# Kernel optimization log

Measured on AMD Instinct MI355X. Metric: run time of the kernel, lower is better.

## Reference

```python
import jax, jax.numpy as jnp
import numpy as np

B, N, F = 4, 1024, 512        # batch, tokens, features
H, D = 8, 64                  # heads, attention_dim (= value dim here)
E = 16                        # edge feature dim
LN_EPS = 1e-5


def setup_inputs() -> dict:
    key = jax.random.key(0)
    ks = jax.random.split(key, 9)
    receiver_input = jax.random.normal(ks[0], (B, N, F), dtype=jnp.float32)
    edge_features = jax.random.normal(ks[1], (B, N, N, E), dtype=jnp.float32)
    mask = (jax.random.uniform(ks[2], (B, N, N)) > 0.5).astype(jnp.float32)
    s = 1.0 / np.sqrt(F)
    Wq = jax.random.normal(ks[3], (F, H * D), dtype=jnp.float32) * s
    Wk = jax.random.normal(ks[4], (F, H * D), dtype=jnp.float32) * s
    Wv = jax.random.normal(ks[5], (F, H * D), dtype=jnp.float32) * s
    We = jax.random.normal(ks[6], (E, H), dtype=jnp.float32) * (1.0 / np.sqrt(E))
    Wo = jax.random.normal(ks[7], (H * D, H * D), dtype=jnp.float32) * (1.0 / np.sqrt(H * D))
    ln_scale = jnp.ones((F,), dtype=jnp.float32)
    ln_offset = jnp.zeros((F,), dtype=jnp.float32)
    return {
        "receiver_input": receiver_input, "edge_features": edge_features,
        "mask": mask, "ln_scale": ln_scale, "ln_offset": ln_offset,
        "Wq": Wq, "Wk": Wk, "Wv": Wv, "We": We, "Wo": Wo,
    }


def _layer_norm(x, scale, offset):
    mu = jnp.mean(x, axis=-1, keepdims=True)
    var = jnp.var(x, axis=-1, keepdims=True)
    return (x - mu) * jax.lax.rsqrt(var + LN_EPS) * scale + offset


def reference(receiver_input, edge_features, mask, ln_scale, ln_offset, Wq, Wk, Wv, We, Wo):
    r = _layer_norm(receiver_input, ln_scale, ln_offset)   # sender = receiver (self-attn)
    q = (r @ Wq).reshape(B, N, H, D)
    k = (r @ Wk).reshape(B, N, H, D)
    v = (r @ Wv).reshape(B, N, H, D)
    # logits [b, i, j, h]; edge bias added BEFORE softmax (over senders j = axis -2)
    logits = jnp.einsum("bihf,bjhf->bijh", q, k) + edge_features @ We
    w = jax.nn.softmax(logits, axis=-2)
    w = w * mask[..., None]                                 # post-softmax mask multiply
    out = jnp.einsum("bijh,bjhv->bihv", w, v)
    out = out.reshape(B, N, H * D) * (1.0 / jnp.sqrt(jnp.float32(D)))
    out = out @ Wo
    out = out + receiver_input                              # residual (shapes match: F == H*D)
    return out
```

## Files before the change

### kernel.cpp

```cpp
#include <hip/hip_runtime.h>

#define BB 4
#define NN 1024
#define FF 512
#define HH 8
#define DD 64
#define EE 16

typedef unsigned short u16;
typedef _Float16 f16;
typedef __attribute__((ext_vector_type(8))) _Float16 f16x8;
typedef __attribute__((ext_vector_type(4))) _Float16 f16x4;
typedef __attribute__((ext_vector_type(4))) float     f32x4;

#define MFMAH(a,b,c) __builtin_amdgcn_mfma_f32_16x16x32_f16((a),(b),(c),0,0,0)

static __device__ __forceinline__ void gld16(const void* g, void* l){
  __builtin_amdgcn_global_load_lds((const __attribute__((address_space(1))) unsigned int*)g,
                                   (__attribute__((address_space(3))) unsigned int*)l, 16, 0, 0);
}

__global__ __launch_bounds__(256) void k_wsplit(
    const float* __restrict__ Wq, const float* __restrict__ Wk,
    const float* __restrict__ Wv, const float* __restrict__ Wo,
    f16* __restrict__ WT, f16* __restrict__ WoT){
  __shared__ float tile[32][33];
  int bid = blockIdx.x, t = threadIdx.x;
  int isA = bid < 768;
  int tb  = isA ? bid : bid - 768;
  int nct = isA ? 48 : 16;
  int ct = tb % nct, ft = tb / nct;
  int c0 = ct * 32, f0 = ft * 32;
  #pragma unroll
  for (int r4 = 0; r4 < 4; r4++){
    int fl = (t >> 5) * 4 + r4, cl = t & 31;
    int f = f0 + fl, c = c0 + cl;
    float v;
    if (isA){
      const float* W = (c < 512) ? Wq : ((c < 1024) ? Wk : Wv);
      v = W[f * 512 + (c & 511)];
    } else {
      v = Wo[f * 512 + c];
    }
    tile[fl][cl] = v;
  }
  __syncthreads();
  #pragma unroll
  for (int r4 = 0; r4 < 4; r4++){
    int cl = (t >> 5) * 4 + r4, fl = t & 31;
    float v = tile[fl][cl];
    int c = c0 + cl, f = f0 + fl;
    if (isA) WT[c * 512 + f]  = (f16)v;
    else     WoT[c * 512 + f] = (f16)v;
  }
}

__global__ __launch_bounds__(256) void k_ln(
    const float* __restrict__ x, const float* __restrict__ gamma,
    const float* __restrict__ beta, f16* __restrict__ rf){
  int row  = blockIdx.x * 4 + (threadIdx.x >> 6);
  int lane = threadIdx.x & 63;
  const float* px = x + (size_t)row * 512 + lane * 8;
  float4 a = *(const float4*)px;
  float4 b = *(const float4*)(px + 4);
  float v[8] = {a.x,a.y,a.z,a.w,b.x,b.y,b.z,b.w};
  float s = 0.f, q = 0.f;
  #pragma unroll
  for (int j = 0; j < 8; j++){ s += v[j]; q += v[j]*v[j]; }
  #pragma unroll
  for (int m = 1; m < 64; m <<= 1){ s += __shfl_xor(s, m, 64); q += __shfl_xor(q, m, 64); }
  float mean = s * (1.f/512.f);
  float var  = q * (1.f/512.f) - mean * mean;
  float rstd = rsqrtf(var + 1e-5f);
  float4 ga = *(const float4*)(gamma + lane*8);
  float4 gb = *(const float4*)(gamma + lane*8 + 4);
  float4 b0 = *(const float4*)(beta  + lane*8);
  float4 b1 = *(const float4*)(beta  + lane*8 + 4);
  float gs[8] = {ga.x,ga.y,ga.z,ga.w,gb.x,gb.y,gb.z,gb.w};
  float bs[8] = {b0.x,b0.y,b0.z,b0.w,b1.x,b1.y,b1.z,b1.w};
  f16x8 hv;
  #pragma unroll
  for (int j = 0; j < 8; j++){
    float r = (v[j] - mean) * rstd * gs[j] + bs[j];
    hv[j] = (f16)r;
  }
  *(f16x8*)(rf + (size_t)row * 512 + lane * 8) = hv;
}

__global__ __launch_bounds__(256) void k_qkv(
    const f16* __restrict__ rf, const f16* __restrict__ WT,
    f16* __restrict__ qf, f16* __restrict__ kf, f16* __restrict__ vT){
  __shared__ f16 As[128*32], Bs[128*32];
  int bid = blockIdx.x;
  int mt = bid & 31, nt = bid >> 5;
  int m0 = mt << 7,  n0 = nt << 7;
  int t = threadIdx.x, lane = t & 63, w = t >> 6;
  int wm = (w >> 1) << 6, wn = (w & 1) << 6;
  int fr = lane & 15, g = lane >> 4;
  f32x4 acc[4][4];
  #pragma unroll
  for (int i = 0; i < 4; i++)
    #pragma unroll
    for (int j = 0; j < 4; j++) acc[i][j] = (f32x4){0.f,0.f,0.f,0.f};

  for (int k0 = 0; k0 < 512; k0 += 32){
    #pragma unroll
    for (int q = 0; q < 2; q++){
      int c = ((q << 2) + w) * 64 + lane;
      int row = c >> 2, part = c & 3;
      int ldso = ((q << 2) + w) * 512;
      gld16(rf + (size_t)(m0+row)*512 + k0 + part*8, &As[ldso]);
      gld16(WT + (size_t)(n0+row)*512 + k0 + part*8, &Bs[ldso]);
    }
    __syncthreads();
    f16x8 a[4], b[4];
    #pragma unroll
    for (int mi = 0; mi < 4; mi++) a[mi] = *(const f16x8*)&As[(wm + mi*16 + fr)*32 + g*8];
    #pragma unroll
    for (int ni = 0; ni < 4; ni++) b[ni] = *(const f16x8*)&Bs[(wn + ni*16 + fr)*32 + g*8];
    #pragma unroll
    for (int mi = 0; mi < 4; mi++)
      #pragma unroll
      for (int ni = 0; ni < 4; ni++)
        acc[mi][ni] = MFMAH(a[mi], b[ni], acc[mi][ni]);
    __syncthreads();
  }
  #pragma unroll
  for (int mi = 0; mi < 4; mi++)
    #pragma unroll
    for (int ni = 0; ni < 4; ni++)
      #pragma unroll
      for (int r = 0; r < 4; r++){
        int gm = m0 + wm + mi*16 + g*4 + r;
        int gc = n0 + wn + ni*16 + fr;
        float vv = acc[mi][ni][r];
        int b = gm >> 10, i = gm & 1023;
        int mat = gc >> 9, h = (gc >> 6) & 7, d = gc & 63;
        size_t idx = ((size_t)((b << 3) + h) * 1024 + i) * 64 + d;
        if      (mat == 0) qf[idx] = (f16)vv;
        else if (mat == 1) kf[idx] = (f16)vv;
        else vT[((size_t)((b << 3) + h) * 64 + d) * 1024 + i] = (f16)vv;
      }
}

__global__ __launch_bounds__(256) void k_bias(
    const float* __restrict__ edge, const float* __restrict__ We,
    f16* __restrict__ biasP){
  int t = threadIdx.x, lane = t & 63, w = t >> 6;
  int c = lane & 3, vq = lane >> 2;
  float wr[4][8];
  #pragma unroll
  for (int r = 0; r < 4; r++){
    float4 wa = *(const float4*)(We + (c*4 + r)*8);
    float4 wb = *(const float4*)(We + (c*4 + r)*8 + 4);
    wr[r][0]=wa.x; wr[r][1]=wa.y; wr[r][2]=wa.z; wr[r][3]=wa.w;
    wr[r][4]=wb.x; wr[r][5]=wb.y; wr[r][6]=wb.z; wr[r][7]=wb.w;
  }
  int bid = blockIdx.x;
  int i = bid & 1023, b = bid >> 10;
  const float* erow = edge + (size_t)bid * 16384;
  f16* obase = biasP + (size_t)(b*8) * 1048576 + (size_t)i * 1024;
  int h0 = 2*c;
  f16* op0 = obase + (size_t)h0 * 1048576;
  f16* op1 = obase + (size_t)(h0 + 1) * 1048576;

  #pragma unroll 2
  for (int n = 0; n < 16; n++){
    int grp = w*16 + n;
    float4 e = *(const float4*)(erow + grp*256 + lane*4);
    float p[8];
    #pragma unroll
    for (int h = 0; h < 8; h++)
      p[h] = e.x*wr[0][h] + e.y*wr[1][h] + e.z*wr[2][h] + e.w*wr[3][h];
    #pragma unroll
    for (int h = 0; h < 8; h++){
      p[h] += __shfl_xor(p[h], 1, 64);
      p[h] += __shfl_xor(p[h], 2, 64);
    }
    int j = grp*16 + vq;
    op0[j] = (f16)p[h0];
    op1[j] = (f16)p[h0 + 1];
  }
}

__global__ __launch_bounds__(256) void k_attn(
    const f16* __restrict__ biasP, const float* __restrict__ mask,
    const f16* __restrict__ qf, const f16* __restrict__ kf,
    const f16* __restrict__ vT, f16* __restrict__ part_o,
    float2* __restrict__ part_md){
  __shared__ f16 pm_s[4][16*40];
  int t = threadIdx.x, lane = t & 63, w = t >> 6;
  int wid = blockIdx.x * 4 + w;
  int s = wid & 1, it = (wid >> 1) & 63, h = (wid >> 7) & 7, b = wid >> 10;
  int fr = lane & 15, g = lane >> 4;
  int bh = b*8 + h;

  size_t qb = ((size_t)bh * 1024 + it*16 + fr) * 64 + g*8;
  f16x8 qf0 = *(const f16x8*)(qf + qb);
  f16x8 qf1 = *(const f16x8*)(qf + qb + 32);

  const f16*   bbase = biasP + ((size_t)bh * 1024 + it*16) * 1024;
  const float* mbase = mask + (size_t)(b*1024 + it*16) * 1024;
  const f16*   kbase = kf + (size_t)bh * 65536;
  const f16*   vbase = vT + (size_t)bh * 65536;

  f32x4 oacc[4];
  #pragma unroll
  for (int vf = 0; vf < 4; vf++) oacc[vf] = (f32x4){0.f,0.f,0.f,0.f};
  float mrun[4], den[4];
  #pragma unroll
  for (int r = 0; r < 4; r++){ mrun[r] = -3e38f; den[r] = 0.f; }

  #pragma unroll 1
  for (int jt = s*16; jt < s*16 + 16; jt++){
    int j0 = jt << 5;
    const f16* kp = kbase + (size_t)(j0 + fr) * 64 + g*8;
    f16x8 kf00 = *(const f16x8*)(kp);
    f16x8 kf01 = *(const f16x8*)(kp + 32);
    f16x8 kf10 = *(const f16x8*)(kp + 16*64);
    f16x8 kf11 = *(const f16x8*)(kp + 16*64 + 32);
    f16x8 vfr[4];
    #pragma unroll
    for (int vf = 0; vf < 4; vf++)
      vfr[vf] = *(const f16x8*)(vbase + (size_t)(vf*16 + fr) * 1024 + j0 + g*8);
    float bs0[4], bs1[4], ms0[4], ms1[4];
    #pragma unroll
    for (int r = 0; r < 4; r++){
      int row = g*4 + r;
      bs0[r] = (float)bbase[(size_t)row*1024 + j0 + fr];
      bs1[r] = (float)bbase[(size_t)row*1024 + j0 + 16 + fr];
      ms0[r] = mbase[(size_t)row*1024 + j0 + fr];
      ms1[r] = mbase[(size_t)row*1024 + j0 + 16 + fr];
    }

    f32x4 lg0 = (f32x4){0.f,0.f,0.f,0.f};
    f32x4 lg1 = (f32x4){0.f,0.f,0.f,0.f};
    lg0 = MFMAH(qf0, kf00, lg0); lg1 = MFMAH(qf0, kf10, lg1);
    lg0 = MFMAH(qf1, kf01, lg0); lg1 = MFMAH(qf1, kf11, lg1);

    float tm[4];
    #pragma unroll
    for (int r = 0; r < 4; r++){
      lg0[r] += bs0[r];
      lg1[r] += bs1[r];
      tm[r] = fmaxf(lg0[r], lg1[r]);
    }
    #pragma unroll
    for (int mk = 1; mk < 16; mk <<= 1){
      #pragma unroll
      for (int r = 0; r < 4; r++) tm[r] = fmaxf(tm[r], __shfl_xor(tm[r], mk, 16));
    }
    float p0[4], p1[4], scl[4], ps[4];
    #pragma unroll
    for (int r = 0; r < 4; r++){
      float nm = fmaxf(mrun[r], tm[r]);
      scl[r] = exp2f((mrun[r] - nm) * 1.44269504089f);
      mrun[r] = nm;
      p0[r] = exp2f((lg0[r] - nm) * 1.44269504089f);
      p1[r] = exp2f((lg1[r] - nm) * 1.44269504089f);
      ps[r] = p0[r] + p1[r];
    }
    #pragma unroll
    for (int mk = 1; mk < 16; mk <<= 1){
      #pragma unroll
      for (int r = 0; r < 4; r++) ps[r] += __shfl_xor(ps[r], mk, 16);
    }
    #pragma unroll
    for (int r = 0; r < 4; r++) den[r] = den[r] * scl[r] + ps[r];
    #pragma unroll
    for (int vf = 0; vf < 4; vf++)
      #pragma unroll
      for (int r = 0; r < 4; r++) oacc[vf][r] *= scl[r];

    #pragma unroll
    for (int r = 0; r < 4; r++){
      int row = g*4 + r;
      pm_s[w][row*40 + fr]      = (f16)(p0[r] * ms0[r]);
      pm_s[w][row*40 + 16 + fr] = (f16)(p1[r] * ms1[r]);
    }
    asm volatile("s_waitcnt lgkmcnt(0)" ::: "memory");
    f16x8 pa = *(const f16x8*)&pm_s[w][fr*40 + g*8];
    #pragma unroll
    for (int vf = 0; vf < 4; vf++)
      oacc[vf] = MFMAH(pa, vfr[vf], oacc[vf]);
  }

  float id[4];
  #pragma unroll
  for (int r = 0; r < 4; r++) id[r] = 1.0f / den[r];
  #pragma unroll
  for (int vf = 0; vf < 4; vf++)
    #pragma unroll
    for (int r = 0; r < 4; r++){
      int row = g*4 + r;
      part_o[((size_t)((s*32 + bh) * 1024) + it*16 + row) * 64 + vf*16 + fr] =
          (f16)(oacc[vf][r] * id[r]);
    }
  if (fr == 0){
    #pragma unroll
    for (int r = 0; r < 4; r++){
      int row = g*4 + r;
      part_md[(size_t)(s*32 + bh) * 1024 + it*16 + row] = make_float2(mrun[r], den[r]);
    }
  }
}

__global__ __launch_bounds__(256) void k_combine(
    const f16* __restrict__ part_o, const float2* __restrict__ part_md,
    f16* __restrict__ AO){
  int wg   = blockIdx.x * 4 + (threadIdx.x >> 6);
  int lane = threadIdx.x & 63;
  int bh = wg >> 10, i = wg & 1023;
  int b = bh >> 3, h = bh & 7;
  float2 md[2];
  float M = -3e38f;
  #pragma unroll
  for (int s = 0; s < 2; s++){
    md[s] = part_md[(size_t)(s*32 + bh) * 1024 + i];
    M = fmaxf(M, md[s].x);
  }
  float wsum = 0.f, o = 0.f;
  #pragma unroll
  for (int s = 0; s < 2; s++){
    float wq = md[s].y * exp2f((md[s].x - M) * 1.44269504089f);
    wsum += wq;
    o += wq * (float)part_o[((size_t)((s*32 + bh) * 1024) + i) * 64 + lane];
  }
  AO[((size_t)(b*1024 + i)) * 512 + h*64 + lane] = (f16)(o * 0.125f / wsum);
}

__global__ __launch_bounds__(256) void k_out(
    const f16* __restrict__ AO, const f16* __restrict__ WoT,
    const float* __restrict__ x, float* __restrict__ out){
  __shared__ f16 As[64*32], Bs[128*32];
  int bid = blockIdx.x;
  int mt = bid & 63, nt = bid >> 6;
  int m0 = mt << 6, n0 = nt << 7;
  int t = threadIdx.x, lane = t & 63, w = t >> 6;
  int wm = (w >> 1) << 5, wn = (w & 1) << 6;
  int fr = lane & 15, g = lane >> 4;
  f32x4 acc[2][4];
  #pragma unroll
  for (int i = 0; i < 2; i++)
    #pragma unroll
    for (int j = 0; j < 4; j++) acc[i][j] = (f32x4){0.f,0.f,0.f,0.f};

  for (int k0 = 0; k0 < 512; k0 += 32){
    {
      int row = t >> 2, part = t & 3;
      gld16(AO + (size_t)(m0+row)*512 + k0 + part*8, &As[w*512]);
    }
    #pragma unroll
    for (int q = 0; q < 2; q++){
      int c = ((q << 2) + w) * 64 + lane;
      int row = c >> 2, part = c & 3;
      gld16(WoT + (size_t)(n0+row)*512 + k0 + part*8, &Bs[((q<<2)+w)*512]);
    }
    __syncthreads();
    f16x8 af[2], bf_[4];
    #pragma unroll
    for (int mi = 0; mi < 2; mi++) af[mi]  = *(const f16x8*)&As[(wm + mi*16 + fr)*32 + g*8];
    #pragma unroll
    for (int ni = 0; ni < 4; ni++) bf_[ni] = *(const f16x8*)&Bs[(wn + ni*16 + fr)*32 + g*8];
    #pragma unroll
    for (int mi = 0; mi < 2; mi++)
      #pragma unroll
      for (int ni = 0; ni < 4; ni++)
        acc[mi][ni] = MFMAH(af[mi], bf_[ni], acc[mi][ni]);
    __syncthreads();
  }
  #pragma unroll
  for (int mi = 0; mi < 2; mi++)
    #pragma unroll
    for (int ni = 0; ni < 4; ni++)
      #pragma unroll
      for (int r = 0; r < 4; r++){
        size_t gm = m0 + wm + mi*16 + g*4 + r;
        size_t gn = n0 + wn + ni*16 + fr;
        out[gm*512 + gn] = acc[mi][ni][r] + x[gm*512 + gn];
      }
}

extern "C" void kernel_launch(void* const* d_in, const int* in_sizes, int n_in,
                              void* d_out, int out_size, void* d_ws, size_t ws_size,
                              hipStream_t stream){
  const float* xin   = (const float*)d_in[0];
  const float* edge  = (const float*)d_in[1];
  const float* mask  = (const float*)d_in[2];
  const float* gamma = (const float*)d_in[3];
  const float* beta  = (const float*)d_in[4];
  const float* Wq    = (const float*)d_in[5];
  const float* Wk    = (const float*)d_in[6];
  const float* Wv    = (const float*)d_in[7];
  const float* We    = (const float*)d_in[8];
  const float* Wo    = (const float*)d_in[9];
  float* out = (float*)d_out;

  f16* p   = (f16*)d_ws;
  f16* WT      = p;   p += 1536*512;
  f16* WoT     = p;   p += 512*512;
  f16* rf      = p;   p += 4096*512;
  f16* qf      = p;   p += 2097152;
  f16* kf      = p;   p += 2097152;
  f16* vT      = p;   p += 2097152;
  f16* biasP   = p;   p += 33554432;
  f16* part_o  = p;   p += 4194304;
  float2* part_md = (float2*)p;
  f16* AO      = rf;

  k_wsplit <<<1024, 256, 0, stream>>>(Wq, Wk, Wv, Wo, WT, WoT);
  k_ln     <<<1024, 256, 0, stream>>>(xin, gamma, beta, rf);
  k_qkv    <<<384,  256, 0, stream>>>(rf, WT, qf, kf, vT);
  k_bias   <<<4096, 256, 0, stream>>>(edge, We, biasP);
  k_attn   <<<1024, 256, 0, stream>>>(biasP, mask, qf, kf, vT, part_o, part_md);
  k_combine<<<8192, 256, 0, stream>>>(part_o, part_md, AO);
  k_out    <<<256,  256, 0, stream>>>(AO, WoT, xin, out);
}
```

Measured before the change: 202.2 us.

## Fuse edge-bias projection into attention kernel, removing biasP intermediate

```diff
diff --git a/kernel.cpp b/kernel.cpp
--- a/kernel.cpp
+++ b/kernel.cpp
@@ -143,66 +143,33 @@
       }
 }
 
-__global__ __launch_bounds__(256) void k_bias(
-    const float* __restrict__ edge, const float* __restrict__ We,
-    f16* __restrict__ biasP){
-  int t = threadIdx.x, lane = t & 63, w = t >> 6;
-  int c = lane & 3, vq = lane >> 2;
-  float wr[4][8];
-  #pragma unroll
-  for (int r = 0; r < 4; r++){
-    float4 wa = *(const float4*)(We + (c*4 + r)*8);
-    float4 wb = *(const float4*)(We + (c*4 + r)*8 + 4);
-    wr[r][0]=wa.x; wr[r][1]=wa.y; wr[r][2]=wa.z; wr[r][3]=wa.w;
-    wr[r][4]=wb.x; wr[r][5]=wb.y; wr[r][6]=wb.z; wr[r][7]=wb.w;
-  }
-  int bid = blockIdx.x;
-  int i = bid & 1023, b = bid >> 10;
-  const float* erow = edge + (size_t)bid * 16384;
-  f16* obase = biasP + (size_t)(b*8) * 1048576 + (size_t)i * 1024;
-  int h0 = 2*c;
-  f16* op0 = obase + (size_t)h0 * 1048576;
-  f16* op1 = obase + (size_t)(h0 + 1) * 1048576;
-
-  #pragma unroll 2
-  for (int n = 0; n < 16; n++){
-    int grp = w*16 + n;
-    float4 e = *(const float4*)(erow + grp*256 + lane*4);
-    float p[8];
-    #pragma unroll
-    for (int h = 0; h < 8; h++)
-      p[h] = e.x*wr[0][h] + e.y*wr[1][h] + e.z*wr[2][h] + e.w*wr[3][h];
-    #pragma unroll
-    for (int h = 0; h < 8; h++){
-      p[h] += __shfl_xor(p[h], 1, 64);
-      p[h] += __shfl_xor(p[h], 2, 64);
-    }
-    int j = grp*16 + vq;
-    op0[j] = (f16)p[h0];
-    op1[j] = (f16)p[h0 + 1];
-  }
-}
-
-__global__ __launch_bounds__(256) void k_attn(
-    const f16* __restrict__ biasP, const float* __restrict__ mask,
+__global__ __launch_bounds__(512) void k_attn(
+    const float* __restrict__ edge, const float* __restrict__ mask,
+    const float* __restrict__ We,
     const f16* __restrict__ qf, const f16* __restrict__ kf,
     const f16* __restrict__ vT, f16* __restrict__ part_o,
     float2* __restrict__ part_md){
-  __shared__ f16 pm_s[4][16*40];
+  __shared__ f16 pm_s[8][16*40];
+  __shared__ u16 biasT[8][2][512];
   int t = threadIdx.x, lane = t & 63, w = t >> 6;
-  int wid = blockIdx.x * 4 + w;
-  int s = wid & 1, it = (wid >> 1) & 63, h = (wid >> 7) & 7, b = wid >> 10;
+  int bid = blockIdx.x;
+  int s = bid & 1, it = (bid >> 1) & 63, b = bid >> 7;
   int fr = lane & 15, g = lane >> 4;
-  int bh = b*8 + h;
+  int bh = b*8 + w;
+  int c = lane & 3, vq = lane >> 2;
+
+  float wc[4];
+  #pragma unroll
+  for (int k = 0; k < 4; k++) wc[k] = We[(c*4 + k)*8 + w];
 
   size_t qb = ((size_t)bh * 1024 + it*16 + fr) * 64 + g*8;
   f16x8 qf0 = *(const f16x8*)(qf + qb);
   f16x8 qf1 = *(const f16x8*)(qf + qb + 32);
 
-  const f16*   bbase = biasP + ((size_t)bh * 1024 + it*16) * 1024;
   const float* mbase = mask + (size_t)(b*1024 + it*16) * 1024;
   const f16*   kbase = kf + (size_t)bh * 65536;
   const f16*   vbase = vT + (size_t)bh * 65536;
+  const float* ebase = edge + ((size_t)(b*1024 + it*16) * 1024 + s*512) * 16;
 
   f32x4 oacc[4];
   #pragma unroll
@@ -212,8 +179,10 @@
   for (int r = 0; r < 4; r++){ mrun[r] = -3e38f; den[r] = 0.f; }
 
   #pragma unroll 1
-  for (int jt = s*16; jt < s*16 + 16; jt++){
-    int j0 = jt << 5;
+  for (int jt = 0; jt < 16; jt++){
+    int j0 = s*512 + (jt << 5);
+    int pb_ = jt & 1;
+
     const f16* kp = kbase + (size_t)(j0 + fr) * 64 + g*8;
     f16x8 kf00 = *(const f16x8*)(kp);
     f16x8 kf01 = *(const f16x8*)(kp + 32);
@@ -223,15 +192,45 @@
     #pragma unroll
     for (int vf = 0; vf < 4; vf++)
       vfr[vf] = *(const f16x8*)(vbase + (size_t)(vf*16 + fr) * 1024 + j0 + g*8);
-    float bs0[4], bs1[4], ms0[4], ms1[4];
+    float ms0[4], ms1[4];
     #pragma unroll
     for (int r = 0; r < 4; r++){
       int row = g*4 + r;
-      bs0[r] = (float)bbase[(size_t)row*1024 + j0 + fr];
-      bs1[r] = (float)bbase[(size_t)row*1024 + j0 + 16 + fr];
       ms0[r] = mbase[(size_t)row*1024 + j0 + fr];
       ms1[r] = mbase[(size_t)row*1024 + j0 + 16 + fr];
     }
+
+    const float* etile = ebase + (size_t)jt * 512;
+    #pragma unroll 1
+    for (int n4 = 0; n4 < 8; n4++){
+      float4 e[4];
+      #pragma unroll
+      for (int m = 0; m < 4; m++){
+        int n = n4*4 + m;
+        e[m] = *(const float4*)(etile + (size_t)(n >> 1)*16384 + (n & 1)*256 + lane*4);
+      }
+      #pragma unroll
+      for (int m = 0; m < 4; m++){
+        int n = n4*4 + m;
+        float pbv = e[m].x*wc[0] + e[m].y*wc[1] + e[m].z*wc[2] + e[m].w*wc[3];
+        pbv += __shfl_xor(pbv, 1, 64);
+        pbv += __shfl_xor(pbv, 2, 64);
+        int v = n*16 + vq;
+        int il = v >> 5, jl = v & 31;
+        int p = ((il >> 2)*16 + (jl & 15))*8 + (jl >> 4)*4 + (il & 3);
+        if (c == 0) biasT[w][pb_][p] = __builtin_bit_cast(u16, (f16)pbv);
+      }
+    }
+    asm volatile("s_waitcnt lgkmcnt(0)" ::: "memory");
+    __builtin_amdgcn_sched_barrier(0);
+
+    float bs0[4], bs1[4];
+    #pragma unroll
+    for (int r = 0; r < 4; r++){
+      bs0[r] = (float)__builtin_bit_cast(f16, biasT[w][pb_][(g*16 + fr)*8 + r]);
+      bs1[r] = (float)__builtin_bit_cast(f16, biasT[w][pb_][(g*16 + fr)*8 + 4 + r]);
+    }
+    __builtin_amdgcn_sched_barrier(0);
 
     f32x4 lg0 = (f32x4){0.f,0.f,0.f,0.f};
     f32x4 lg1 = (f32x4){0.f,0.f,0.f,0.f};
@@ -279,6 +278,7 @@
       pm_s[w][row*40 + 16 + fr] = (f16)(p1[r] * ms1[r]);
     }
     asm volatile("s_waitcnt lgkmcnt(0)" ::: "memory");
+    __builtin_amdgcn_sched_barrier(0);
     f16x8 pa = *(const f16x8*)&pm_s[w][fr*40 + g*8];
     #pragma unroll
     for (int vf = 0; vf < 4; vf++)
@@ -403,7 +403,6 @@
   f16* qf      = p;   p += 2097152;
   f16* kf      = p;   p += 2097152;
   f16* vT      = p;   p += 2097152;
-  f16* biasP   = p;   p += 33554432;
   f16* part_o  = p;   p += 4194304;
   float2* part_md = (float2*)p;
   f16* AO      = rf;
@@ -411,8 +410,7 @@
   k_wsplit <<<1024, 256, 0, stream>>>(Wq, Wk, Wv, Wo, WT, WoT);
   k_ln     <<<1024, 256, 0, stream>>>(xin, gamma, beta, rf);
   k_qkv    <<<384,  256, 0, stream>>>(rf, WT, qf, kf, vT);
-  k_bias   <<<4096, 256, 0, stream>>>(edge, We, biasP);
-  k_attn   <<<1024, 256, 0, stream>>>(biasP, mask, qf, kf, vT, part_o, part_md);
+  k_attn   <<<512,  512, 0, stream>>>(edge, mask, We, qf, kf, vT, part_o, part_md);
   k_combine<<<8192, 256, 0, stream>>>(part_o, part_md, AO);
   k_out    <<<256,  256, 0, stream>>>(AO, WoT, xin, out);
 }
```

After: 247.2 us. +22.2%, slower.
